# Performance work log

Measured on AMD Instinct MI355X. Metric: run time of the kernel, lower is better.

## Reference

```python
import jax, jax.numpy as jnp
import numpy as np

B, N, D_IN, D_OUT = 32, 256, 512, 2048
RANK, K, H_CTRL = 12, 16, 192
RESIDUAL_SCALE = 1.0


def setup_inputs() -> dict:
    key = jax.random.key(0)
    ks = jax.random.split(key, 12)
    x = jax.random.normal(ks[0], (B, N, D_IN), dtype=jnp.float32)
    shared_weight = 0.02 * jax.random.normal(ks[1], (D_OUT, D_IN), dtype=jnp.float32)
    bias = jnp.zeros((D_OUT,), dtype=jnp.float32)
    # orthogonal init for U_0 [out, in] via QR of a Gaussian
    g = jax.random.normal(ks[2], (D_OUT, D_IN), dtype=jnp.float32)
    U0, _ = jnp.linalg.qr(g, mode='reduced')  # columns orthonormal, out>=in
    left_basis = 0.02 * jax.random.normal(ks[3], (K, D_OUT, RANK), dtype=jnp.float32)
    right_basis = 0.02 * jax.random.normal(ks[4], (K, D_IN, RANK), dtype=jnp.float32)
    ctrl_dim = 3 * D_IN  # cls_mean_var pooling
    W1 = (1.0 / np.sqrt(ctrl_dim)) * jax.random.normal(ks[5], (ctrl_dim, H_CTRL), dtype=jnp.float32)
    b1 = jnp.zeros((H_CTRL,), dtype=jnp.float32)
    Wc = (1.0 / np.sqrt(H_CTRL)) * jax.random.normal(ks[6], (H_CTRL, K), dtype=jnp.float32)
    bc = jnp.zeros((K,), dtype=jnp.float32)
    Wg = (1.0 / np.sqrt(H_CTRL)) * jax.random.normal(ks[7], (H_CTRL, 1), dtype=jnp.float32)
    bg = jnp.zeros((1,), dtype=jnp.float32)
    return {"x": x, "shared_weight": shared_weight, "bias": bias, "U0": U0,
            "left_basis": left_basis, "right_basis": right_basis,
            "W1": W1, "b1": b1, "Wc": Wc, "bc": bc, "Wg": Wg, "bg": bg}


def _controller(z, W1, b1, Wc, bc, Wg, bg):
    # MLP controller: coeff head (linear) + gate head (sigmoid)
    h = jax.nn.gelu(z @ W1 + b1)
    coeff = h @ Wc + bc            # [B, K]
    gate = jax.nn.sigmoid(h @ Wg + bg)  # [B, 1]
    return coeff, gate


def reference(x, shared_weight, bias, U0, left_basis, right_basis, W1, b1, Wc, bc, Wg, bg):
    # conditioning signal: cls + mean + var (unbiased=False)
    cls = x[:, 0]
    mean = x.mean(axis=1)
    var = x.var(axis=1)  # population variance, matches unbiased=False
    z = jnp.concatenate([cls, mean, var], axis=-1)  # [B, 3*D_IN]
    coeff, gate = _controller(z, W1, b1, Wc, bc, Wg, bg)

    # tangent dictionary
    raw = jnp.einsum('kmr,kdr->kmd', left_basis, right_basis)        # [K, M, D]
    ut_raw = jnp.einsum('mi,kmj->kij', U0, raw)                       # U0^T @ raw: [K, D, D]
    sym = 0.5 * (ut_raw + jnp.swapaxes(ut_raw, -2, -1))
    tangent = raw - jnp.einsum('mi,kij->kmj', U0, sym)                # [K, M, D]
    norm = jnp.sqrt(jnp.sum(tangent * tangent, axis=(1, 2), keepdims=True))
    tangent = tangent / jnp.maximum(norm, 1e-6)

    # per-sample candidate + QR retraction (Stiefel)
    delta = jnp.einsum('bk,kmd->bmd', coeff, tangent)                 # [B, M, D]
    candidate = U0[None] + RESIDUAL_SCALE * delta
    q, r = jnp.linalg.qr(candidate, mode='reduced')                   # q: [B, M, D]
    sign = jnp.sign(jnp.diagonal(r, axis1=-2, axis2=-1))              # [B, D]
    sign = jnp.where(sign == 0, jnp.ones_like(sign), sign)
    dynamic_weight = q * sign[..., None, :]
    residual_weight = dynamic_weight - U0[None]                       # [B, M, D]

    out = x @ shared_weight.T + bias                                  # [B, N, M]
    residual_out = jnp.einsum('bnd,bmd->bnm', x, residual_weight)     # [B, N, M]
    return out + gate.reshape(-1, 1, 1) * residual_out
```

## Files before the change

kernel.cpp:

```cpp
#include <hip/hip_runtime.h>
#include <math.h>

#define B_    32
#define N_    256
#define DIN   512
#define DOUT  2048
#define RANK_ 12
#define K_    16
#define HC    192
#define CD    1536
#define P1    192
#define P2    384

typedef short short8 __attribute__((ext_vector_type(8)));
typedef float f32x4 __attribute__((ext_vector_type(4)));

__device__ inline short bf16r(float f) {
  unsigned u = __float_as_uint(f);
  unsigned r = (u + 0x7FFFu + ((u >> 16) & 1u)) >> 16;
  return (short)r;
}
__device__ inline float b16f(short s) {
  unsigned u = ((unsigned)(unsigned short)s) << 16;
  return __uint_as_float(u);
}

__global__ __launch_bounds__(256) void k_pre1(const float* __restrict__ x,
                                              const float* __restrict__ leftb,
                                              const float* __restrict__ rightb,
                                              float* __restrict__ sp, float* __restrict__ s2p,
                                              float* __restrict__ Lcat, float* __restrict__ E) {
  int bx = blockIdx.x, t = threadIdx.x;
  if (bx < 256) {
    int b = bx >> 3, c = bx & 7;
    const float* xb = x + (size_t)b * N_ * DIN;
#pragma unroll
    for (int h2 = 0; h2 < 2; ++h2) {
      int d = t + h2 * 256;
      float s = 0.f, s2 = 0.f;
      for (int n = c * 32; n < c * 32 + 32; ++n) {
        float v = xb[(size_t)n * DIN + d];
        s += v; s2 += v * v;
      }
      sp[(size_t)(b * 8 + c) * DIN + d] = s;
      s2p[(size_t)(b * 8 + c) * DIN + d] = s2;
    }
  } else {
    int idx = (bx - 256) * 256 + t;
    const int totL = DOUT * P1;
    const int totR = DIN * P1;
    if (idx < totL) {
      int m = idx / P1, j = idx - m * P1;
      int k = j / RANK_, r = j - k * RANK_;
      Lcat[idx] = leftb[((size_t)k * DOUT + m) * RANK_ + r];
    } else if (idx < totL + totR) {
      int i2 = idx - totL;
      int d = i2 / P1, j = i2 - d * P1;
      int k = j / RANK_, r = j - k * RANK_;
      E[(size_t)d * P2 + j] = rightb[((size_t)k * DIN + d) * RANK_ + r];
    }
  }
}

__device__ inline void gemm_tn_part(const float* __restrict__ A, const float* __restrict__ B,
                                    float* __restrict__ C, int i0, int j0, int kb0, int klen,
                                    int lda, int ldb, int ldc,
                                    float (*As)[33], float (*Bs)[33], int t) {
  int ii = t & 31, j4 = (t >> 5) * 4;
  float acc[4] = {0.f, 0.f, 0.f, 0.f};
  for (int kb = kb0; kb < kb0 + klen; kb += 32) {
    for (int idx = t; idx < 1024; idx += 256) {
      int kk = idx >> 5, c = idx & 31;
      As[kk][c] = A[(size_t)(kb + kk) * lda + i0 + c];
      Bs[kk][c] = B[(size_t)(kb + kk) * ldb + j0 + c];
    }
    __syncthreads();
#pragma unroll 8
    for (int kk = 0; kk < 32; ++kk) {
      float a = As[kk][ii];
#pragma unroll
      for (int q = 0; q < 4; ++q) acc[q] = fmaf(a, Bs[kk][j4 + q], acc[q]);
    }
    __syncthreads();
  }
#pragma unroll
  for (int q = 0; q < 4; ++q) C[(size_t)(i0 + ii) * ldc + j0 + j4 + q] = acc[q];
}

__global__ __launch_bounds__(256) void k_pre2(const float* __restrict__ x,
                                              const float* __restrict__ sp, const float* __restrict__ s2p,
                                              const float* __restrict__ W1, const float* __restrict__ b1,
                                              const float* __restrict__ U0, const float* __restrict__ LcatF,
                                              float* __restrict__ hgel,
                                              float* __restrict__ Ppart, float* __restrict__ GLLpart) {
  int bx = blockIdx.x, t = threadIdx.x;
  __shared__ float As[32][33], Bs[32][33];
  __shared__ float zsh[CD];
  __shared__ float hp[4][64];
  if (bx < 96) {
    int b = bx / 3, jt = bx % 3;
    int j0 = jt * 64;
    for (int d = t; d < CD; d += 256) {
      float v;
      if (d < DIN) {
        v = x[(size_t)b * N_ * DIN + d];
      } else {
        int dd = d & 511;
        float s = 0.f;
#pragma unroll
        for (int c2 = 0; c2 < 8; ++c2) s += sp[(size_t)(b * 8 + c2) * DIN + dd];
        float mean = s * (1.0f / N_);
        if (d < 2 * DIN) v = mean;
        else {
          float s2 = 0.f;
#pragma unroll
          for (int c2 = 0; c2 < 8; ++c2) s2 += s2p[(size_t)(b * 8 + c2) * DIN + dd];
          v = s2 * (1.0f / N_) - mean * mean;
        }
      }
      zsh[d] = v;
    }
    __syncthreads();
    int j = t & 63, kg = t >> 6;
    float a = 0.f;
    for (int d = kg * 384; d < kg * 384 + 384; ++d)
      a = fmaf(zsh[d], W1[(size_t)d * HC + j0 + j], a);
    hp[kg][j] = a;
    __syncthreads();
    if (kg == 0) {
      float acc = hp[0][j] + hp[1][j] + hp[2][j] + hp[3][j] + b1[j0 + j];
      float x3 = acc * acc * acc;
      float hj = 0.5f * acc * (1.0f + tanhf(0.7978845608028654f * (acc + 0.044715f * x3)));
      hgel[b * HC + j0 + j] = hj;
    }
  } else if (bx < 480) {
    int pb = bx - 96;
    int tile = pb % 96, ks = pb / 96;
    gemm_tn_part(U0, LcatF, Ppart + (size_t)ks * 98304, (tile & 15) * 32, (tile >> 4) * 32,
                 ks * 512, 512, DIN, P1, P1, As, Bs, t);
  } else {
    int gb = bx - 480;
    int tile = gb % 36, ks = gb / 36;
    gemm_tn_part(LcatF, LcatF, GLLpart + (size_t)ks * 36864, (tile % 6) * 32, (tile / 6) * 32,
                 ks * 512, 512, P1, P1, P1, As, Bs, t);
  }
}

__global__ __launch_bounds__(256) void k_pre2b(const float* __restrict__ Ppart,
                                               const float* __restrict__ GLLpart,
                                               float* __restrict__ E, float* __restrict__ GLL) {
  int idx = blockIdx.x * 256 + threadIdx.x;
  if (idx < 98304) {
    float s = Ppart[idx] + Ppart[98304 + idx] + Ppart[2 * 98304 + idx] + Ppart[3 * 98304 + idx];
    int d = idx / P1, j = idx - d * P1;
    E[(size_t)d * P2 + P1 + j] = s;
  } else if (idx < 98304 + 36864) {
    int i2 = idx - 98304;
    GLL[i2] = GLLpart[i2] + GLLpart[36864 + i2] + GLLpart[2 * 36864 + i2] + GLLpart[3 * 36864 + i2];
  }
}

__global__ __launch_bounds__(256) void k_pre3(const float* __restrict__ E,
                                              const float* __restrict__ Wsh, const float* __restrict__ U0,
                                              const float* __restrict__ LcatF,
                                              float* __restrict__ GE, short* __restrict__ Bcat,
                                              short* __restrict__ Eb16, short* __restrict__ Etb16) {
  int bx = blockIdx.x, t = threadIdx.x;
  __shared__ float As[32][33], Bs[32][33];
  if (bx < 144) {
    gemm_tn_part(E, E, GE, (bx % 12) * 32, (bx / 12) * 32, 0, DIN, P2, P2, P2, As, Bs, t);
  } else if (bx < 1360) {
    int idx = (bx - 144) * 256 + t;
    int row = idx / 152, g = idx - row * 152;
    const float* src;
    if (g < 64)       src = Wsh + (size_t)row * DIN + g * 8;
    else if (g < 128) src = U0 + (size_t)row * DIN + (g - 64) * 8;
    else              src = LcatF + (size_t)row * P1 + (g - 128) * 8;
    short8 o;
#pragma unroll
    for (int e = 0; e < 8; ++e) o[e] = bf16r(src[e]);
    *(short8*)(Bcat + (size_t)row * 1216 + g * 8) = o;
  } else {
    int idx = (bx - 1360) * 256 + t;
    int d = idx / P2, q = idx - d * P2;
    short v = bf16r(E[idx]);
    Eb16[idx] = v;
    Etb16[(size_t)q * DIN + d] = v;
  }
}

__global__ __launch_bounds__(512) void k_pre4(const float* __restrict__ GLL, const float* __restrict__ GE,
                                              const float* __restrict__ hgel,
                                              const float* __restrict__ Wc, const float* __restrict__ bc,
                                              const float* __restrict__ Wg, const float* __restrict__ bg,
                                              float* __restrict__ gate, float* __restrict__ cp) {
  __shared__ float nrm[16];
  int t = threadIdx.x;
  int k = t >> 5, lane = t & 31;
  float s1 = 0.f, s2 = 0.f, s3 = 0.f;
  for (int idx = lane; idx < RANK_ * RANK_; idx += 32) {
    int r = idx / RANK_, s = idx - r * RANK_;
    int p = k * RANK_ + r, q = k * RANK_ + s;
    float gll = GLL[p * P1 + q];
    float grr = GE[p * P2 + q];
    float gpp = GE[(P1 + p) * P2 + (P1 + q)];
    float gpr = GE[(P1 + p) * P2 + q];
    float gprt = GE[(P1 + q) * P2 + p];
    s1 += gll * grr;
    s2 += gpp * grr;
    s3 += gpr * gprt;
  }
#pragma unroll
  for (int off = 16; off > 0; off >>= 1) {
    s1 += __shfl_down(s1, off, 32);
    s2 += __shfl_down(s2, off, 32);
    s3 += __shfl_down(s3, off, 32);
  }
  if (lane == 0) nrm[k] = sqrtf(fmaxf(s1 - 0.5f * (s2 + s3), 0.0f));
  int bb = t >> 4, kk = t & 15;
  float c = bc[kk];
  const float* hb = hgel + bb * HC;
  for (int q = 0; q < HC; ++q) c = fmaf(hb[q], Wc[q * K_ + kk], c);
  if (t < B_) {
    float g = bg[0];
    const float* hb2 = hgel + t * HC;
    for (int q = 0; q < HC; ++q) g = fmaf(hb2[q], Wg[q], g);
    gate[t] = 1.0f / (1.0f + expf(-g));
  }
  __syncthreads();
  cp[t] = c / fmaxf(nrm[kk], 1e-6f);
}

__global__ __launch_bounds__(256) void k_pre5(const float* __restrict__ GLL, const float* __restrict__ GE,
                                              const float* __restrict__ E, const float* __restrict__ cp,
                                              short* __restrict__ M0b, short* __restrict__ Ecb) {
  int bx = blockIdx.x, t = threadIdx.x;
  if (bx < 576) {
    int idx = bx * 256 + t;
    if (idx >= P2 * P2) return;
    int p = idx / P2, q = idx - p * P2;
    float v;
    if (p < P1) {
      if (q < P1) v = GLL[p * P1 + q] - 0.75f * GE[(P1 + p) * P2 + (P1 + q)];
      else        v = -0.25f * GE[(P1 + p) * P2 + (q - P1)];
    } else {
      if (q < P1) v = -0.25f * GE[(P1 + q) * P2 + (p - P1)];
      else        v = 0.25f * GE[(p - P1) * P2 + (q - P1)];
    }
    M0b[idx] = bf16r(v);
  } else {
    int idx = (bx - 576) * 256 + t;
    int b = idx / (DIN * 48);
    int rem = idx - b * DIN * 48;
    int d = rem / 48, g = rem - d * 48;
    int q0 = g * 8;
    const float* src = E + (size_t)d * P2 + q0;
    const float* cpb = cp + b * K_;
    short8 o;
#pragma unroll
    for (int e = 0; e < 8; ++e) {
      int q = q0 + e;
      int kidx = (q % P1) / RANK_;
      o[e] = bf16r(src[e] * cpb[kidx]);
    }
    *(short8*)(Ecb + ((size_t)b * DIN + d) * P2 + q0) = o;
  }
}

template<int MSZ, int NSZ, int KD>
__global__ __launch_bounds__(256) void k_mf_nt16(const short* __restrict__ A,
                                                 const short* __restrict__ B,
                                                 short* __restrict__ C) {
  int b = blockIdx.z;
  const short* Ab = A + (size_t)b * MSZ * KD;
  short* Cb = C + (size_t)b * MSZ * NSZ;
  int c0 = blockIdx.x * 64, r0 = blockIdx.y * 64;
  __shared__ short As[64][40], Bs[64][40];
  int t = threadIdx.x;
  int l = t & 63, wid = t >> 6;
  int wr = wid >> 1, wc = wid & 1;
  int fr = l & 15, fq = l >> 4;
  int row = t >> 2, cg = t & 3;
  f32x4 acc[2][2] = {};
  for (int kt = 0; kt < KD / 32; ++kt) {
    *(short8*)&As[row][cg * 8] = *(const short8*)(Ab + (size_t)(r0 + row) * KD + kt * 32 + cg * 8);
    *(short8*)&Bs[row][cg * 8] = *(const short8*)(B + (size_t)(c0 + row) * KD + kt * 32 + cg * 8);
    __syncthreads();
    short8 af[2], bf[2];
#pragma unroll
    for (int m = 0; m < 2; ++m) af[m] = *(const short8*)&As[wr * 32 + m * 16 + fr][fq * 8];
#pragma unroll
    for (int n = 0; n < 2; ++n) bf[n] = *(const short8*)&Bs[wc * 32 + n * 16 + fr][fq * 8];
#pragma unroll
    for (int m = 0; m < 2; ++m)
#pragma unroll
      for (int n = 0; n < 2; ++n)
        acc[m][n] = __builtin_amdgcn_mfma_f32_16x16x32_bf16(af[m], bf[n], acc[m][n], 0, 0, 0);
    __syncthreads();
  }
#pragma unroll
  for (int m = 0; m < 2; ++m)
#pragma unroll
    for (int n = 0; n < 2; ++n)
#pragma unroll
      for (int j = 0; j < 4; ++j)
        Cb[(size_t)(r0 + wr * 32 + m * 16 + fq * 4 + j) * NSZ + c0 + wc * 32 + n * 16 + fr] =
            bf16r(acc[m][n][j]);
}

__global__ __launch_bounds__(256) void k_mf_G(const short* __restrict__ H,
                                              const short* __restrict__ Ec,
                                              float* __restrict__ G) {
  int b = blockIdx.z;
  const short* Ab = H + (size_t)b * DIN * P2;
  const short* Bb = Ec + (size_t)b * DIN * P2;
  float* Gb = G + (size_t)b * DIN * DIN;
  int c0 = blockIdx.x * 64, r0 = blockIdx.y * 64;
  __shared__ short As[64][40], Bs[64][40];
  int t = threadIdx.x;
  int l = t & 63, wid = t >> 6;
  int wr = wid >> 1, wc = wid & 1;
  int fr = l & 15, fq = l >> 4;
  int row = t >> 2, cg = t & 3;
  f32x4 acc[2][2] = {};
  for (int kt = 0; kt < P2 / 32; ++kt) {
    *(short8*)&As[row][cg * 8] = *(const short8*)(Ab + (size_t)(r0 + row) * P2 + kt * 32 + cg * 8);
    *(short8*)&Bs[row][cg * 8] = *(const short8*)(Bb + (size_t)(c0 + row) * P2 + kt * 32 + cg * 8);
    __syncthreads();
    short8 af[2], bf[2];
#pragma unroll
    for (int m = 0; m < 2; ++m) af[m] = *(const short8*)&As[wr * 32 + m * 16 + fr][fq * 8];
#pragma unroll
    for (int n = 0; n < 2; ++n) bf[n] = *(const short8*)&Bs[wc * 32 + n * 16 + fr][fq * 8];
#pragma unroll
    for (int m = 0; m < 2; ++m)
#pragma unroll
      for (int n = 0; n < 2; ++n)
        acc[m][n] = __builtin_amdgcn_mfma_f32_16x16x32_bf16(af[m], bf[n], acc[m][n], 0, 0, 0);
    __syncthreads();
  }
#pragma unroll
  for (int m = 0; m < 2; ++m)
#pragma unroll
    for (int n = 0; n < 2; ++n)
#pragma unroll
      for (int j = 0; j < 4; ++j) {
        int gr = r0 + wr * 32 + m * 16 + fq * 4 + j;
        int gc = c0 + wc * 32 + n * 16 + fr;
        Gb[(size_t)gr * DIN + gc] = acc[m][n][j] + (gr == gc ? 1.0f : 0.0f);
      }
}

__global__ __launch_bounds__(64) void k_chol_dp2(float* __restrict__ G, float* __restrict__ Wd,
                                                 int j0) {
  int b = blockIdx.y;
  int role = blockIdx.x;
  float* Gb = G + (size_t)b * DIN * DIN;
  __shared__ float D[64][65];
  __shared__ float Wls[64][65];
  __shared__ float dinvs[64];
  int t = threadIdx.x;
#pragma unroll 8
  for (int i = 0; i < 64; ++i) D[i][t] = Gb[(size_t)(j0 + i) * DIN + j0 + t];
  __syncthreads();
  {
    float col[64];
#pragma unroll
    for (int i = 0; i < 64; ++i) col[i] = D[i][t];
#pragma unroll
    for (int j = 0; j < 64; ++j) {
      float djj = __shfl(col[j], j);
      float rjj = sqrtf(fmaxf(djj, 1e-30f));
      float rinv = 1.0f / rjj;
      if (t == j) col[j] = rjj;
      else if (t > j) col[j] *= rinv;
      float djt = col[j];
#pragma unroll
      for (int i = j + 1; i < 64; ++i) {
        float rji = __shfl(col[j], i);
        if (i <= t) col[i] = fmaf(-rji, djt, col[i]);
      }
    }
#pragma unroll
    for (int i = 0; i < 64; ++i) D[i][t] = (i <= t) ? col[i] : 0.0f;
    dinvs[t] = 1.0f / col[t];
  }
  __syncthreads();
  if (role == 0) {
#pragma unroll 4
    for (int i = 0; i < 64; ++i) Wls[i][t] = 0.0f;
    Wls[t][t] = dinvs[t];
    for (int i = 62; i >= 0; --i) {
      float s = 0.0f;
      for (int j = i + 1; j < 64; ++j) s = fmaf(D[i][j], Wls[j][t], s);
      if (t > i) Wls[i][t] = -s * dinvs[i];
    }
    float* Wp = Wd + ((size_t)b * 8 + (j0 >> 6)) * 4096;
#pragma unroll 4
    for (int i = 0; i < 64; ++i) Wp[i * 64 + t] = Wls[i][t];
  } else {
    int c = j0 + 64 + (role - 1) * 64 + t;
    float a[64];
#pragma unroll
    for (int i = 0; i < 64; ++i) a[i] = Gb[(size_t)(j0 + i) * DIN + c];
#pragma unroll
    for (int j = 0; j < 64; ++j) {
      float aj = a[j] * dinvs[j];
      a[j] = aj;
#pragma unroll
      for (int i = j + 1; i < 64; ++i) a[i] = fmaf(-D[j][i], aj, a[i]);
    }
#pragma unroll
    for (int i = 0; i < 64; ++i) Gb[(size_t)(j0 + i) * DIN + c] = a[i];
  }
}

__global__ __launch_bounds__(256) void k_chol_tr(float* __restrict__ G, int j0, int nt) {
  int b = blockIdx.y;
  int pi = blockIdx.x;
  int ti = 0, accum = 0;
  while (pi >= accum + (nt - ti)) { accum += nt - ti; ++ti; }
  int tc = ti + (pi - accum);
  float* Gb = G + (size_t)b * DIN * DIN;
  __shared__ float As[64][65], Bs[64][65];
  int t = threadIdx.x;
  int ibase = j0 + 64 + ti * 64, cbase = j0 + 64 + tc * 64;
  for (int idx = t; idx < 4096; idx += 256) {
    int j = idx >> 6, c = idx & 63;
    As[j][c] = Gb[(size_t)(j0 + j) * DIN + ibase + c];
    Bs[j][c] = Gb[(size_t)(j0 + j) * DIN + cbase + c];
  }
  __syncthreads();
  int tx = t & 15, ty = t >> 4;
  float acc[4][4] = {};
#pragma unroll 8
  for (int k = 0; k < 64; ++k) {
    float a[4], bv[4];
#pragma unroll
    for (int u = 0; u < 4; ++u) a[u] = As[k][ty * 4 + u];
#pragma unroll
    for (int v = 0; v < 4; ++v) bv[v] = Bs[k][tx * 4 + v];
#pragma unroll
    for (int u = 0; u < 4; ++u)
#pragma unroll
      for (int v = 0; v < 4; ++v) acc[u][v] = fmaf(a[u], bv[v], acc[u][v]);
  }
#pragma unroll
  for (int u = 0; u < 4; ++u) {
    size_t ro = (size_t)(ibase + ty * 4 + u) * DIN + cbase + tx * 4;
#pragma unroll
    for (int v = 0; v < 4; ++v) Gb[ro + v] -= acc[u][v];
  }
}

__global__ __launch_bounds__(256) void k_trif(const float* __restrict__ x, const float* __restrict__ G,
                                              const float* __restrict__ Wd, short* __restrict__ ybf,
                                              short* __restrict__ ycb) {
  int b = blockIdx.y;
  int n0 = blockIdx.x * 32;
  const float* R = G + (size_t)b * DIN * DIN;
  const float* xb = x + ((size_t)b * N_ + n0) * DIN;
  __shared__ float Yl[32][513];
  __shared__ float Rs[64][65];
  __shared__ float Wds[64][65];
  __shared__ float Ytmp[32][65];
  int t = threadIdx.x;
  for (int idx = t; idx < 32 * DIN; idx += 256)
    Yl[idx >> 9][idx & 511] = xb[(size_t)(idx >> 9) * DIN + (idx & 511)];
  __syncthreads();
  int r = t & 31, cg = t >> 5;
  for (int p = 7; p >= 0; --p) {
    int j0 = p * 64;
    int kN = DIN - j0 - 64;
    float acc[8] = {};
    for (int kb = 0; kb < kN; kb += 64) {
      for (int idx = t; idx < 4096; idx += 256) {
        int kk = idx & 63, c = idx >> 6;
        Rs[kk][c] = R[(size_t)(j0 + c) * DIN + j0 + 64 + kb + kk];
      }
      __syncthreads();
#pragma unroll 8
      for (int kk = 0; kk < 64; ++kk) {
        float a = Yl[r][j0 + 64 + kb + kk];
#pragma unroll
        for (int v = 0; v < 8; ++v) acc[v] = fmaf(a, Rs[kk][cg * 8 + v], acc[v]);
      }
      __syncthreads();
    }
#pragma unroll
    for (int v = 0; v < 8; ++v) Ytmp[r][cg * 8 + v] = Yl[r][j0 + cg * 8 + v] - acc[v];
    const float* Wp = Wd + ((size_t)b * 8 + p) * 4096;
    for (int idx = t; idx < 4096; idx += 256) Wds[idx >> 6][idx & 63] = Wp[idx];
    __syncthreads();
    float o[8] = {};
#pragma unroll 8
    for (int jj = 0; jj < 64; ++jj) {
      float a = Ytmp[r][jj];
#pragma unroll
      for (int v = 0; v < 8; ++v) o[v] = fmaf(a, Wds[cg * 8 + v][jj], o[v]);
    }
    __syncthreads();
#pragma unroll
    for (int v = 0; v < 8; ++v) Yl[r][j0 + cg * 8 + v] = o[v];
    __syncthreads();
  }
  for (int idx = t; idx < 32 * DIN; idx += 256) {
    int rr = idx >> 9, c = idx & 511;
    float yv = Yl[rr][c];
    float xv = xb[(size_t)rr * DIN + c];
    size_t gi = ((size_t)b * N_ + n0 + rr) * DIN + c;
    ybf[gi] = bf16r(yv);
    ycb[gi] = bf16r(yv - xv);
  }
}

__global__ __launch_bounds__(256) void k_yEuv(const short* __restrict__ A,
                                              const short* __restrict__ B,
                                              const float* __restrict__ cp,
                                              const float* __restrict__ gate,
                                              short* __restrict__ C, short* __restrict__ vb) {
  int b = blockIdx.z;
  const short* Ab = A + (size_t)b * N_ * DIN;
  short* Cb = C + (size_t)b * N_ * P2;
  int c0 = blockIdx.x * 64, r0 = blockIdx.y * 64;
  __shared__ short As[64][40], Bs[64][40];
  __shared__ float cps[K_];
  int t = threadIdx.x;
  if (t < K_) cps[t] = cp[b * K_ + t];
  int l = t & 63, wid = t >> 6;
  int wr = wid >> 1, wc = wid & 1;
  int fr = l & 15, fq = l >> 4;
  int row = t >> 2, cg = t & 3;
  f32x4 acc[2][2] = {};
  __syncthreads();
  for (int kt = 0; kt < DIN / 32; ++kt) {
    *(short8*)&As[row][cg * 8] = *(const short8*)(Ab + (size_t)(r0 + row) * DIN + kt * 32 + cg * 8);
    *(short8*)&Bs[row][cg * 8] = *(const short8*)(B + (size_t)(c0 + row) * DIN + kt * 32 + cg * 8);
    __syncthreads();
    short8 af[2], bf[2];
#pragma unroll
    for (int m = 0; m < 2; ++m) af[m] = *(const short8*)&As[wr * 32 + m * 16 + fr][fq * 8];
#pragma unroll
    for (int n = 0; n < 2; ++n) bf[n] = *(const short8*)&Bs[wc * 32 + n * 16 + fr][fq * 8];
#pragma unroll
    for (int m = 0; m < 2; ++m)
#pragma unroll
      for (int n = 0; n < 2; ++n)
        acc[m][n] = __builtin_amdgcn_mfma_f32_16x16x32_bf16(af[m], bf[n], acc[m][n], 0, 0, 0);
    __syncthreads();
  }
  float gt = gate[b];
#pragma unroll
  for (int m = 0; m < 2; ++m)
#pragma unroll
    for (int n = 0; n < 2; ++n)
#pragma unroll
      for (int j = 0; j < 4; ++j) {
        int gr = r0 + wr * 32 + m * 16 + fq * 4 + j;
        int gc = c0 + wc * 32 + n * 16 + fr;
        float v = acc[m][n][j];
        Cb[(size_t)gr * P2 + gc] = bf16r(v);
        if (gc < P1)
          vb[((size_t)b * N_ + gr) * P1 + gc] = bf16r(gt * cps[gc / RANK_] * v);
      }
}

__global__ __launch_bounds__(256) void k_mf_w(const short* __restrict__ yE16,
                                              const short* __restrict__ Eb,
                                              const short* __restrict__ ycb,
                                              const float* __restrict__ cp,
                                              const float* __restrict__ gate,
                                              short* __restrict__ wb) {
  int b = blockIdx.z;
  const short* yEb = yE16 + (size_t)b * N_ * P2;
  int c0 = blockIdx.x * 64, r0 = blockIdx.y * 64;
  __shared__ short As[64][40], Bs[64][40];
  __shared__ float cps[K_];
  int t = threadIdx.x;
  if (t < K_) cps[t] = 0.5f * cp[b * K_ + t];
  int l = t & 63, wid = t >> 6;
  int wr = wid >> 1, wc = wid & 1;
  int fr = l & 15, fq = l >> 4;
  int row = t >> 2, cg = t & 3;
  f32x4 acc[2][2] = {};
  __syncthreads();
  for (int kt = 0; kt < P2 / 32; ++kt) {
    int ksrc0 = (kt * 32 + P1) % P2;
    short8 raw = *(const short8*)(yEb + (size_t)(r0 + row) * P2 + ksrc0 + cg * 8);
    short8 oa;
#pragma unroll
    for (int e = 0; e < 8; ++e) {
      int q = kt * 32 + cg * 8 + e;
      int kidx = (q % P1) / RANK_;
      oa[e] = bf16r(b16f(raw[e]) * cps[kidx]);
    }
    *(short8*)&As[row][cg * 8] = oa;
    *(short8*)&Bs[row][cg * 8] = *(const short8*)(Eb + (size_t)(c0 + row) * P2 + kt * 32 + cg * 8);
    __syncthreads();
    short8 af[2], bf[2];
#pragma unroll
    for (int m = 0; m < 2; ++m) af[m] = *(const short8*)&As[wr * 32 + m * 16 + fr][fq * 8];
#pragma unroll
    for (int n = 0; n < 2; ++n) bf[n] = *(const short8*)&Bs[wc * 32 + n * 16 + fr][fq * 8];
#pragma unroll
    for (int m = 0; m < 2; ++m)
#pragma unroll
      for (int n = 0; n < 2; ++n)
        acc[m][n] = __builtin_amdgcn_mfma_f32_16x16x32_bf16(af[m], bf[n], acc[m][n], 0, 0, 0);
    __syncthreads();
  }
  float gt = gate[b];
#pragma unroll
  for (int m = 0; m < 2; ++m)
#pragma unroll
    for (int n = 0; n < 2; ++n)
#pragma unroll
      for (int j = 0; j < 4; ++j) {
        int gr = r0 + wr * 32 + m * 16 + fq * 4 + j;
        int gc = c0 + wc * 32 + n * 16 + fr;
        size_t gi = ((size_t)b * N_ + gr) * DIN + gc;
        wb[gi] = bf16r(gt * (b16f(ycb[gi]) - acc[m][n][j]));
      }
}

__device__ inline short8 loadA8(const float* __restrict__ x, const short* __restrict__ wb,
                                const short* __restrict__ vb, int grow, int k0) {
  if (k0 < 512) {
    const float* p = x + (size_t)grow * 512 + k0;
    float4 f0 = *(const float4*)p;
    float4 f1 = *(const float4*)(p + 4);
    short8 o;
    o[0] = bf16r(f0.x); o[1] = bf16r(f0.y); o[2] = bf16r(f0.z); o[3] = bf16r(f0.w);
    o[4] = bf16r(f1.x); o[5] = bf16r(f1.y); o[6] = bf16r(f1.z); o[7] = bf16r(f1.w);
    return o;
  } else if (k0 < 1024) {
    return *(const short8*)(wb + (size_t)grow * 512 + k0 - 512);
  } else {
    return *(const short8*)(vb + (size_t)grow * 192 + k0 - 1024);
  }
}

__global__ __launch_bounds__(256) void k_final(
    const float* __restrict__ x, const short* __restrict__ wb, const short* __restrict__ vb,
    const short* __restrict__ Bcat, const float* __restrict__ bias, float* __restrict__ out) {
  __shared__ short As[2][4096];
  __shared__ short Bs[2][4096];
  int t = threadIdx.x;
  int c0 = blockIdx.x * 128;
  int r0 = blockIdx.y * 128;
  int l = t & 63, wid = t >> 6;
  int wr = wid >> 1, wc = wid & 1;
  int fr = l & 15, fq = l >> 4;
  f32x4 acc[4][4] = {};
  short8 ra0, ra1, rb0, rb1;
  const int row0 = t >> 2, c8 = t & 3;
  const int row1 = row0 + 64;
  ra0 = loadA8(x, wb, vb, r0 + row0, c8 * 8);
  ra1 = loadA8(x, wb, vb, r0 + row1, c8 * 8);
  rb0 = *(const short8*)(Bcat + (size_t)(c0 + row0) * 1216 + c8 * 8);
  rb1 = *(const short8*)(Bcat + (size_t)(c0 + row1) * 1216 + c8 * 8);
  *(short8*)&As[0][row0 * 32 + c8 * 8] = ra0;
  *(short8*)&As[0][row1 * 32 + c8 * 8] = ra1;
  *(short8*)&Bs[0][row0 * 32 + c8 * 8] = rb0;
  *(short8*)&Bs[0][row1 * 32 + c8 * 8] = rb1;
  __syncthreads();
  for (int kt = 0; kt < 38; ++kt) {
    int cur = kt & 1;
    if (kt + 1 < 38) {
      int k0 = (kt + 1) * 32;
      ra0 = loadA8(x, wb, vb, r0 + row0, k0 + c8 * 8);
      ra1 = loadA8(x, wb, vb, r0 + row1, k0 + c8 * 8);
      rb0 = *(const short8*)(Bcat + (size_t)(c0 + row0) * 1216 + k0 + c8 * 8);
      rb1 = *(const short8*)(Bcat + (size_t)(c0 + row1) * 1216 + k0 + c8 * 8);
    }
    short8 af[4], bf[4];
#pragma unroll
    for (int m = 0; m < 4; ++m)
      af[m] = *(const short8*)&As[cur][(wr * 64 + m * 16 + fr) * 32 + fq * 8];
#pragma unroll
    for (int n = 0; n < 4; ++n)
      bf[n] = *(const short8*)&Bs[cur][(wc * 64 + n * 16 + fr) * 32 + fq * 8];
#pragma unroll
    for (int m = 0; m < 4; ++m)
#pragma unroll
      for (int n = 0; n < 4; ++n)
        acc[m][n] = __builtin_amdgcn_mfma_f32_16x16x32_bf16(af[m], bf[n], acc[m][n], 0, 0, 0);
    __syncthreads();
    if (kt + 1 < 38) {
      int nxt = cur ^ 1;
      *(short8*)&As[nxt][row0 * 32 + c8 * 8] = ra0;
      *(short8*)&As[nxt][row1 * 32 + c8 * 8] = ra1;
      *(short8*)&Bs[nxt][row0 * 32 + c8 * 8] = rb0;
      *(short8*)&Bs[nxt][row1 * 32 + c8 * 8] = rb1;
    }
    __syncthreads();
  }
#pragma unroll
  for (int n = 0; n < 4; ++n) {
    int col = c0 + wc * 64 + n * 16 + fr;
    float bv = bias[col];
#pragma unroll
    for (int m = 0; m < 4; ++m) {
      int rbase = r0 + wr * 64 + m * 16 + fq * 4;
#pragma unroll
      for (int j = 0; j < 4; ++j)
        out[(size_t)(rbase + j) * DOUT + col] = acc[m][n][j] + bv;
    }
  }
}

extern "C" void kernel_launch(void* const* d_in, const int* in_sizes, int n_in,
                              void* d_out, int out_size, void* d_ws, size_t ws_size,
                              hipStream_t stream) {
  (void)in_sizes; (void)n_in; (void)out_size; (void)ws_size;
  const float* x     = (const float*)d_in[0];
  const float* Wsh   = (const float*)d_in[1];
  const float* bias  = (const float*)d_in[2];
  const float* U0    = (const float*)d_in[3];
  const float* leftb = (const float*)d_in[4];
  const float* rightb= (const float*)d_in[5];
  const float* W1    = (const float*)d_in[6];
  const float* b1    = (const float*)d_in[7];
  const float* Wc    = (const float*)d_in[8];
  const float* bc    = (const float*)d_in[9];
  const float* Wg    = (const float*)d_in[10];
  const float* bg    = (const float*)d_in[11];
  float* out = (float*)d_out;

  float* wsf = (float*)d_ws;
  float* hgel  = wsf + 0;
  float* gate  = wsf + 49664;
  float* cp    = wsf + 49792;
  float* LcatF = wsf + 50304;
  float* E     = wsf + 443520;
  float* GLL   = wsf + 640128;
  float* GE    = wsf + 676992;
  short* M0b16 = (short*)(wsf + 824448);
  short* Eb16  = (short*)(wsf + 898176);
  short* Etb16 = (short*)(wsf + 996480);
  short* wb    = (short*)(wsf + 1094784);
  short* Ecb   = (short*)(wsf + 3191936);
  short* ybf   = (short*)(wsf + 3191936);
  short* vb    = (short*)(wsf + 5289088);
  short* Hb16  = (short*)(wsf + 6337664);
  short* ycb   = (short*)(wsf + 6337664);
  short* Bcat  = (short*)(wsf + 9483392);
  float* sp      = wsf + 10728576;
  float* s2p     = wsf + 10859648;
  float* Ppart   = wsf + 10990720;
  float* GLLpart = wsf + 11383936;
  float* G = out;
  float* Wd = out + 8388608;
  short* yE16 = (short*)(out + 8388608 + 1048576);

  k_pre1<<<256 + 1920, 256, 0, stream>>>(x, leftb, rightb, sp, s2p, LcatF, E);
  k_pre2<<<624, 256, 0, stream>>>(x, sp, s2p, W1, b1, U0, LcatF, hgel, Ppart, GLLpart);
  k_pre2b<<<528, 256, 0, stream>>>(Ppart, GLLpart, E, GLL);
  k_pre3<<<2128, 256, 0, stream>>>(E, Wsh, U0, LcatF, GE, Bcat, Eb16, Etb16);
  k_pre4<<<1, 512, 0, stream>>>(GLL, GE, hgel, Wc, bc, Wg, bg, gate, cp);
  k_pre5<<<3648, 256, 0, stream>>>(GLL, GE, E, cp, M0b16, Ecb);
  k_mf_nt16<DIN, P2, P2><<<dim3(P2 / 64, DIN / 64, B_), 256, 0, stream>>>(Ecb, M0b16, Hb16);
  k_mf_G<<<dim3(DIN / 64, DIN / 64, B_), 256, 0, stream>>>(Hb16, Ecb, G);
  for (int p = 0; p < 8; ++p) {
    int j0 = p * 64;
    int nt = 7 - p;
    k_chol_dp2<<<dim3(nt + 1, B_), 64, 0, stream>>>(G, Wd, j0);
    if (nt > 0)
      k_chol_tr<<<dim3(nt * (nt + 1) / 2, B_), 256, 0, stream>>>(G, j0, nt);
  }
  k_trif<<<dim3(N_ / 32, B_), 256, 0, stream>>>(x, G, Wd, ybf, ycb);
  k_yEuv<<<dim3(P2 / 64, N_ / 64, B_), 256, 0, stream>>>(ybf, Etb16, cp, gate, yE16, vb);
  k_mf_w<<<dim3(DIN / 64, N_ / 64, B_), 256, 0, stream>>>(yE16, Eb16, ycb, cp, gate, wb);
  k_final<<<dim3(DOUT / 128, (B_ * N_) / 128), 256, 0, stream>>>(x, wb, vb, Bcat, bias, out);
}
```

Before: 1.534 ms.

## Switch blocked Cholesky to left-looking form and halve trif row tile

```diff
diff --git a/kernel.cpp b/kernel.cpp
--- a/kernel.cpp
+++ b/kernel.cpp
@@ -351,19 +351,59 @@
       }
 }
 
-__global__ __launch_bounds__(64) void k_chol_dp2(float* __restrict__ G, float* __restrict__ Wd,
-                                                 int j0) {
+__global__ __launch_bounds__(256) void k_chol_lp(float* __restrict__ G, float* __restrict__ Wd,
+                                                 int p) {
   int b = blockIdx.y;
   int role = blockIdx.x;
   float* Gb = G + (size_t)b * DIN * DIN;
+  int j0 = p * 64;
   __shared__ float D[64][65];
-  __shared__ float Wls[64][65];
+  __shared__ float As[64][65];
+  __shared__ float Bs[64][65];
   __shared__ float dinvs[64];
   int t = threadIdx.x;
+  int tx = t & 15, ty = t >> 4;
+  int c0 = j0 + 64 + (role - 1) * 64;
+  float accD[4][4] = {};
+  float accC[4][4] = {};
+  for (int q = 0; q < p; ++q) {
+    for (int idx = t; idx < 4096; idx += 256) {
+      int i = idx >> 6, c = idx & 63;
+      As[i][c] = Gb[(size_t)(q * 64 + i) * DIN + j0 + c];
+      if (role > 0) Bs[i][c] = Gb[(size_t)(q * 64 + i) * DIN + c0 + c];
+    }
+    __syncthreads();
 #pragma unroll 8
-  for (int i = 0; i < 64; ++i) D[i][t] = Gb[(size_t)(j0 + i) * DIN + j0 + t];
+    for (int k = 0; k < 64; ++k) {
+      float a[4], bd[4];
+#pragma unroll
+      for (int u = 0; u < 4; ++u) a[u] = As[k][ty * 4 + u];
+#pragma unroll
+      for (int v = 0; v < 4; ++v) bd[v] = As[k][tx * 4 + v];
+#pragma unroll
+      for (int u = 0; u < 4; ++u)
+#pragma unroll
+        for (int v = 0; v < 4; ++v) accD[u][v] = fmaf(a[u], bd[v], accD[u][v]);
+      if (role > 0) {
+        float bc2[4];
+#pragma unroll
+        for (int v = 0; v < 4; ++v) bc2[v] = Bs[k][tx * 4 + v];
+#pragma unroll
+        for (int u = 0; u < 4; ++u)
+#pragma unroll
+          for (int v = 0; v < 4; ++v) accC[u][v] = fmaf(a[u], bc2[v], accC[u][v]);
+      }
+    }
+    __syncthreads();
+  }
+#pragma unroll
+  for (int u = 0; u < 4; ++u)
+#pragma unroll
+    for (int v = 0; v < 4; ++v)
+      D[ty * 4 + u][tx * 4 + v] =
+          Gb[(size_t)(j0 + ty * 4 + u) * DIN + j0 + tx * 4 + v] - accD[u][v];
   __syncthreads();
-  {
+  if (t < 64) {
     float col[64];
 #pragma unroll
     for (int i = 0; i < 64; ++i) col[i] = D[i][t];
@@ -387,69 +427,41 @@
   }
   __syncthreads();
   if (role == 0) {
+    if (t < 64) {
 #pragma unroll 4
-    for (int i = 0; i < 64; ++i) Wls[i][t] = 0.0f;
-    Wls[t][t] = dinvs[t];
-    for (int i = 62; i >= 0; --i) {
-      float s = 0.0f;
-      for (int j = i + 1; j < 64; ++j) s = fmaf(D[i][j], Wls[j][t], s);
-      if (t > i) Wls[i][t] = -s * dinvs[i];
-    }
-    float* Wp = Wd + ((size_t)b * 8 + (j0 >> 6)) * 4096;
+      for (int i = 0; i < 64; ++i) Bs[i][t] = 0.0f;
+      Bs[t][t] = dinvs[t];
+      for (int i = 62; i >= 0; --i) {
+        float s = 0.0f;
+        for (int j = i + 1; j < 64; ++j) s = fmaf(D[i][j], Bs[j][t], s);
+        if (t > i) Bs[i][t] = -s * dinvs[i];
+      }
+      float* Wp = Wd + ((size_t)b * 8 + p) * 4096;
 #pragma unroll 4
-    for (int i = 0; i < 64; ++i) Wp[i * 64 + t] = Wls[i][t];
+      for (int i = 0; i < 64; ++i) Wp[i * 64 + t] = Bs[i][t];
+    }
   } else {
-    int c = j0 + 64 + (role - 1) * 64 + t;
-    float a[64];
-#pragma unroll
-    for (int i = 0; i < 64; ++i) a[i] = Gb[(size_t)(j0 + i) * DIN + c];
-#pragma unroll
-    for (int j = 0; j < 64; ++j) {
-      float aj = a[j] * dinvs[j];
-      a[j] = aj;
-#pragma unroll
-      for (int i = j + 1; i < 64; ++i) a[i] = fmaf(-D[j][i], aj, a[i]);
-    }
-#pragma unroll
-    for (int i = 0; i < 64; ++i) Gb[(size_t)(j0 + i) * DIN + c] = a[i];
-  }
-}
-
-__global__ __launch_bounds__(256) void k_chol_tr(float* __restrict__ G, int j0, int nt) {
-  int b = blockIdx.y;
-  int pi = blockIdx.x;
-  int ti = 0, accum = 0;
-  while (pi >= accum + (nt - ti)) { accum += nt - ti; ++ti; }
-  int tc = ti + (pi - accum);
-  float* Gb = G + (size_t)b * DIN * DIN;
-  __shared__ float As[64][65], Bs[64][65];
-  int t = threadIdx.x;
-  int ibase = j0 + 64 + ti * 64, cbase = j0 + 64 + tc * 64;
-  for (int idx = t; idx < 4096; idx += 256) {
-    int j = idx >> 6, c = idx & 63;
-    As[j][c] = Gb[(size_t)(j0 + j) * DIN + ibase + c];
-    Bs[j][c] = Gb[(size_t)(j0 + j) * DIN + cbase + c];
-  }
-  __syncthreads();
-  int tx = t & 15, ty = t >> 4;
-  float acc[4][4] = {};
-#pragma unroll 8
-  for (int k = 0; k < 64; ++k) {
-    float a[4], bv[4];
-#pragma unroll
-    for (int u = 0; u < 4; ++u) a[u] = As[k][ty * 4 + u];
-#pragma unroll
-    for (int v = 0; v < 4; ++v) bv[v] = Bs[k][tx * 4 + v];
 #pragma unroll
     for (int u = 0; u < 4; ++u)
 #pragma unroll
-      for (int v = 0; v < 4; ++v) acc[u][v] = fmaf(a[u], bv[v], acc[u][v]);
-  }
-#pragma unroll
-  for (int u = 0; u < 4; ++u) {
-    size_t ro = (size_t)(ibase + ty * 4 + u) * DIN + cbase + tx * 4;
-#pragma unroll
-    for (int v = 0; v < 4; ++v) Gb[ro + v] -= acc[u][v];
+      for (int v = 0; v < 4; ++v)
+        Bs[ty * 4 + u][tx * 4 + v] =
+            Gb[(size_t)(j0 + ty * 4 + u) * DIN + c0 + tx * 4 + v] - accC[u][v];
+    __syncthreads();
+    if (t < 64) {
+      float a[64];
+#pragma unroll
+      for (int i = 0; i < 64; ++i) a[i] = Bs[i][t];
+#pragma unroll
+      for (int j = 0; j < 64; ++j) {
+        float aj = a[j] * dinvs[j];
+        a[j] = aj;
+#pragma unroll
+        for (int i = j + 1; i < 64; ++i) a[i] = fmaf(-D[j][i], aj, a[i]);
+      }
+#pragma unroll
+      for (int i = 0; i < 64; ++i) Gb[(size_t)(j0 + i) * DIN + c0 + t] = a[i];
+    }
   }
 }
 
@@ -457,22 +469,22 @@
                                               const float* __restrict__ Wd, short* __restrict__ ybf,
                                               short* __restrict__ ycb) {
   int b = blockIdx.y;
-  int n0 = blockIdx.x * 32;
+  int n0 = blockIdx.x * 16;
   const float* R = G + (size_t)b * DIN * DIN;
   const float* xb = x + ((size_t)b * N_ + n0) * DIN;
-  __shared__ float Yl[32][513];
+  __shared__ float Yl[16][517];
   __shared__ float Rs[64][65];
   __shared__ float Wds[64][65];
-  __shared__ float Ytmp[32][65];
+  __shared__ float Ytmp[16][69];
   int t = threadIdx.x;
-  for (int idx = t; idx < 32 * DIN; idx += 256)
+  for (int idx = t; idx < 16 * DIN; idx += 256)
     Yl[idx >> 9][idx & 511] = xb[(size_t)(idx >> 9) * DIN + (idx & 511)];
   __syncthreads();
-  int r = t & 31, cg = t >> 5;
+  int r = t & 15, cg = t >> 4;
   for (int p = 7; p >= 0; --p) {
     int j0 = p * 64;
     int kN = DIN - j0 - 64;
-    float acc[8] = {};
+    float acc[4] = {0.f, 0.f, 0.f, 0.f};
     for (int kb = 0; kb < kN; kb += 64) {
       for (int idx = t; idx < 4096; idx += 256) {
         int kk = idx & 63, c = idx >> 6;
@@ -483,28 +495,28 @@
       for (int kk = 0; kk < 64; ++kk) {
         float a = Yl[r][j0 + 64 + kb + kk];
 #pragma unroll
-        for (int v = 0; v < 8; ++v) acc[v] = fmaf(a, Rs[kk][cg * 8 + v], acc[v]);
+        for (int v = 0; v < 4; ++v) acc[v] = fmaf(a, Rs[kk][cg * 4 + v], acc[v]);
       }
       __syncthreads();
     }
 #pragma unroll
-    for (int v = 0; v < 8; ++v) Ytmp[r][cg * 8 + v] = Yl[r][j0 + cg * 8 + v] - acc[v];
+    for (int v = 0; v < 4; ++v) Ytmp[r][cg * 4 + v] = Yl[r][j0 + cg * 4 + v] - acc[v];
     const float* Wp = Wd + ((size_t)b * 8 + p) * 4096;
     for (int idx = t; idx < 4096; idx += 256) Wds[idx >> 6][idx & 63] = Wp[idx];
     __syncthreads();
-    float o[8] = {};
+    float o[4] = {0.f, 0.f, 0.f, 0.f};
 #pragma unroll 8
     for (int jj = 0; jj < 64; ++jj) {
       float a = Ytmp[r][jj];
 #pragma unroll
-      for (int v = 0; v < 8; ++v) o[v] = fmaf(a, Wds[cg * 8 + v][jj], o[v]);
-    }
-    __syncthreads();
-#pragma unroll
-    for (int v = 0; v < 8; ++v) Yl[r][j0 + cg * 8 + v] = o[v];
-    __syncthreads();
-  }
-  for (int idx = t; idx < 32 * DIN; idx += 256) {
+      for (int v = 0; v < 4; ++v) o[v] = fmaf(a, Wds[cg * 4 + v][jj], o[v]);
+    }
+    __syncthreads();
+#pragma unroll
+    for (int v = 0; v < 4; ++v) Yl[r][j0 + cg * 4 + v] = o[v];
+    __syncthreads();
+  }
+  for (int idx = t; idx < 16 * DIN; idx += 256) {
     int rr = idx >> 9, c = idx & 511;
     float yv = Yl[rr][c];
     float xv = xb[(size_t)rr * DIN + c];
@@ -761,14 +773,9 @@
   k_pre5<<<3648, 256, 0, stream>>>(GLL, GE, E, cp, M0b16, Ecb);
   k_mf_nt16<DIN, P2, P2><<<dim3(P2 / 64, DIN / 64, B_), 256, 0, stream>>>(Ecb, M0b16, Hb16);
   k_mf_G<<<dim3(DIN / 64, DIN / 64, B_), 256, 0, stream>>>(Hb16, Ecb, G);
-  for (int p = 0; p < 8; ++p) {
-    int j0 = p * 64;
-    int nt = 7 - p;
-    k_chol_dp2<<<dim3(nt + 1, B_), 64, 0, stream>>>(G, Wd, j0);
-    if (nt > 0)
-      k_chol_tr<<<dim3(nt * (nt + 1) / 2, B_), 256, 0, stream>>>(G, j0, nt);
-  }
-  k_trif<<<dim3(N_ / 32, B_), 256, 0, stream>>>(x, G, Wd, ybf, ycb);
+  for (int p = 0; p < 8; ++p)
+    k_chol_lp<<<dim3(8 - p, B_), 256, 0, stream>>>(G, Wd, p);
+  k_trif<<<dim3(N_ / 16, B_), 256, 0, stream>>>(x, G, Wd, ybf, ycb);
   k_yEuv<<<dim3(P2 / 64, N_ / 64, B_), 256, 0, stream>>>(ybf, Etb16, cp, gate, yE16, vb);
   k_mf_w<<<dim3(DIN / 64, N_ / 64, B_), 256, 0, stream>>>(yE16, Eb16, ycb, cp, gate, wb);
   k_final<<<dim3(DOUT / 128, (B_ * N_) / 128), 256, 0, stream>>>(x, wb, vb, Bcat, bias, out);
```

New measurement: 1.650 ms. 7.5% more time.
